# Kernel tuning notes

Hardware: AMD Instinct MI355X
Metric: run time of the kernel (lower is better)

## Reference

```python
import jax, jax.numpy as jnp
import numpy as np

N = 50000      # nodes
E = 800000     # edges (before self loops)
F_IN = 512     # input feature dim (num_features)
D = 128        # hidden_dim
NBLK = 3       # num_layers - 1
EPS = 1e-5


def _layernorm(x, g, b):
    mu = x.mean(-1, keepdims=True)
    var = ((x - mu) ** 2).mean(-1, keepdims=True)
    return (x - mu) / jnp.sqrt(var + EPS) * g + b


def _gatv2(x, Wl, bl, Wr, br, att, bias, src, dst, n):
    # PyG GATv2Conv, heads=1, eval mode (attention dropout off), self loops in src/dst
    xl = x @ Wl + bl                      # [N, D] messages (x_j side)
    xr = x @ Wr + br                      # [N, D] target side (x_i)
    e = jax.nn.leaky_relu(xl[src] + xr[dst], negative_slope=0.2)  # [E', D]
    score = e @ att                       # [E']
    smax = jax.ops.segment_max(score, dst, num_segments=n)
    ex = jnp.exp(score - smax[dst])
    denom = jax.ops.segment_sum(ex, dst, num_segments=n)
    alpha = ex / denom[dst]               # segment softmax over incoming edges
    out = jax.ops.segment_sum(alpha[:, None] * xl[src], dst, num_segments=n)
    return out + bias


def setup_inputs() -> dict:
    key = jax.random.key(0)
    ks = jax.random.split(key, 32)
    w = lambda k, shape: (jax.random.normal(k, shape, jnp.float32) * 0.02)
    p = {}
    p["x"] = jax.random.normal(ks[0], (N, F_IN), jnp.float32)
    p["edge_index"] = jax.random.randint(ks[1], (2, E), 0, N)
    p["emb_W"] = w(ks[2], (F_IN, D)); p["emb_b"] = jnp.zeros((D,), jnp.float32)
    p["ln1_g"] = jnp.ones((NBLK, D), jnp.float32); p["ln1_b"] = jnp.zeros((NBLK, D), jnp.float32)
    p["gat_Wl"] = w(ks[3], (NBLK, D, D)); p["gat_bl"] = jnp.zeros((NBLK, D), jnp.float32)
    p["gat_Wr"] = w(ks[4], (NBLK, D, D)); p["gat_br"] = jnp.zeros((NBLK, D), jnp.float32)
    p["gat_att"] = w(ks[5], (NBLK, D)); p["gat_bias"] = jnp.zeros((NBLK, D), jnp.float32)
    for i in range(NBLK):
        h = D * (i + 1)  # mlp_ratio = level = i+1
        p[f"mlp_w1_{i}"] = w(ks[6 + 2 * i], (D, h))
        p[f"mlp_w2_{i}"] = w(ks[7 + 2 * i], (h, D))
    p["attn_Wa"] = w(ks[12], (D, D)); p["attn_ba"] = jnp.zeros((D,), jnp.float32)
    p["attn_Wb"] = w(ks[13], (D, D)); p["attn_bb"] = jnp.zeros((D,), jnp.float32)
    p["attn_Wc"] = w(ks[14], (D, 1)); p["attn_bc"] = jnp.zeros((1,), jnp.float32)
    p["rho_W"] = w(ks[15], (D, D)); p["rho_b"] = jnp.zeros((D,), jnp.float32)
    p["cls_W"] = w(ks[16], (D, 4)); p["cls_b"] = jnp.zeros((4,), jnp.float32)
    return p


def reference(x, edge_index, emb_W, emb_b, ln1_g, ln1_b, gat_Wl, gat_bl, gat_Wr, gat_br,
              gat_att, gat_bias, mlp_w1_0, mlp_w2_0, mlp_w1_1, mlp_w2_1, mlp_w1_2, mlp_w2_2,
              attn_Wa, attn_ba, attn_Wb, attn_bb, attn_Wc, attn_bc, rho_W, rho_b, cls_W, cls_b):
    n = x.shape[0]
    sl = jnp.arange(n, dtype=edge_index.dtype)
    src = jnp.concatenate([edge_index[0], sl])  # add self loops (GATv2Conv default)
    dst = jnp.concatenate([edge_index[1], sl])
    h = jax.nn.relu(x @ emb_W + emb_b)          # embedding (dropout off)
    mlps = [(mlp_w1_0, mlp_w2_0), (mlp_w1_1, mlp_w2_1), (mlp_w1_2, mlp_w2_2)]
    for i in range(NBLK):
        hn = _layernorm(h, ln1_g[i], ln1_b[i])
        h = h + _gatv2(hn, gat_Wl[i], gat_bl[i], gat_Wr[i], gat_br[i], gat_att[i], gat_bias[i], src, dst, n)
        w1, w2 = mlps[i]
        # NOTE: original forward applies channel_mix directly on x (norm2 is unused)
        h = h + jax.nn.gelu(h @ w1, approximate=False) @ w2
    # Attn_Net_Gated pooling
    a = jnp.tanh(h @ attn_Wa + attn_ba)
    b = jax.nn.sigmoid(h @ attn_Wb + attn_bb)
    A = ((a * b) @ attn_Wc + attn_bc).T          # [1, N]
    h_path = jax.nn.softmax(A, axis=1) @ h       # [1, D]
    hr = jax.nn.relu(h_path @ rho_W + rho_b)
    logits = hr @ cls_W + cls_b                  # [1, 4]
    Y_hat = jnp.argmax(logits, axis=1, keepdims=True)
    hazards = jax.nn.sigmoid(logits)
    S = jnp.cumprod(1.0 - hazards, axis=1)
    return (hazards, S, Y_hat, logits)
```

## Files before the change

### kernel.cpp

```cpp
#include <hip/hip_runtime.h>
#include <math.h>


#define D 128
#define NBLK 3

typedef __attribute__((ext_vector_type(8))) short bf16x8;
typedef __attribute__((ext_vector_type(4))) float f32x4;

static __device__ __forceinline__ float wred_sum(float v) {
#pragma unroll
    for (int m = 1; m < 64; m <<= 1) v += __shfl_xor(v, m, 64);
    return v;
}

static __device__ __forceinline__ float bf2f(unsigned short u) {
    union { unsigned i; float f; } c; c.i = ((unsigned)u) << 16; return c.f;
}
static __device__ __forceinline__ unsigned short f2bf(float f) {
    union { float f; unsigned i; } c; c.f = f;
    unsigned r = c.i + 0x7fff + ((c.i >> 16) & 1);
    return (unsigned short)(r >> 16);
}

static __device__ __forceinline__ void gl16(const unsigned short* g, unsigned short* l) {
    __builtin_amdgcn_global_load_lds((const __attribute__((address_space(1))) void*)g,
                                     (__attribute__((address_space(3))) void*)l, 16, 0, 0);
}

__global__ void zero_k(int* deg, int* fill, float* red, int n) {
    int i = blockIdx.x * blockDim.x + threadIdx.x;
    if (i < n) { deg[i] = 0; fill[i] = 0; }
    if (i < 132) red[i] = 0.f;
}

__global__ void hist_k(const int* __restrict__ dst, int* __restrict__ deg, int E) {
    int e = blockIdx.x * blockDim.x + threadIdx.x;
    if (e < E) atomicAdd(&deg[dst[e]], 1);
}

__global__ __launch_bounds__(256) void blockscan_k(const int* __restrict__ deg,
                                                   int* __restrict__ rowptr,
                                                   int* __restrict__ bsum, int n) {
    __shared__ int tmp[256];
    const int tid = threadIdx.x;
    const int i = blockIdx.x * 256 + tid;
    int v = (i < n) ? deg[i] : 0;
    tmp[tid] = v;
    __syncthreads();
#pragma unroll
    for (int off = 1; off < 256; off <<= 1) {
        int t = (tid >= off) ? tmp[tid - off] : 0;
        __syncthreads();
        tmp[tid] += t;
        __syncthreads();
    }
    if (i < n) rowptr[i + 1] = tmp[tid];
    if (tid == 255) bsum[blockIdx.x] = tmp[255];
}

__global__ __launch_bounds__(256) void scansums_k(int* __restrict__ bsum, int nb) {
    __shared__ int tmp[256];
    const int tid = threadIdx.x;
    int v = (tid < nb) ? bsum[tid] : 0;
    tmp[tid] = v;
    __syncthreads();
#pragma unroll
    for (int off = 1; off < 256; off <<= 1) {
        int t = (tid >= off) ? tmp[tid - off] : 0;
        __syncthreads();
        tmp[tid] += t;
        __syncthreads();
    }
    if (tid < nb) bsum[tid] = tmp[tid];
}

__global__ __launch_bounds__(256) void addoff_k(int* __restrict__ rowptr,
                                                const int* __restrict__ bsum, int n) {
    int i = blockIdx.x * 256 + threadIdx.x;
    if (i == 0) rowptr[0] = 0;
    if (i < n && blockIdx.x > 0) rowptr[i + 1] += bsum[blockIdx.x - 1];
}

__global__ void scatter_k(const int* __restrict__ src, const int* __restrict__ dst,
                          const int* __restrict__ rowptr, int* __restrict__ fill,
                          int* __restrict__ esrc, int E) {
    int e = blockIdx.x * blockDim.x + threadIdx.x;
    if (e < E) {
        int d = dst[e];
        int pos = rowptr[d] + atomicAdd(&fill[d], 1);
        esrc[pos] = src[e];
    }
}

struct WDesc { const float* s; unsigned short* d; int K; int M; };
struct WPack { WDesc w[16]; };

__global__ __launch_bounds__(256) void wprep_k(WPack p) {
    WDesc d = p.w[blockIdx.y];
    const int nc = d.K / 32;
    const int chunks = (d.M / 16) * nc * 64;
    for (int i = blockIdx.x * 256 + threadIdx.x; i < chunks; i += gridDim.x * 256) {
        const int l = i & 63;
        const int c = (i >> 6) % nc;
        const int t = i / (64 * nc);
        const int m = t * 16 + (l & 15);
        const int kb = c * 32 + ((l >> 4) & 3) * 8;
#pragma unroll
        for (int j = 0; j < 8; ++j)
            d.d[(size_t)i * 8 + j] = f2bf(d.s[(size_t)(kb + j) * d.M + m]);
    }
}

__global__ __launch_bounds__(256) void bcat_k(const float* bl, const float* br,
                                              const float* ba, const float* bb,
                                              float* sb) {
    const int t = threadIdx.x;
    for (int i = 0; i < 3; ++i)
        sb[i * 256 + t] = (t < 128) ? bl[i * 128 + t] : br[i * 128 + t - 128];
    sb[3 * 256 + t] = (t < 128) ? ba[t] : bb[t - 128];
}

template <int TK, int TBN, int ACT, bool BIAS, bool ACC, bool LNM, bool A16,
          bool W32, bool W16>
__global__ __launch_bounds__(256) void rgemm_k(const void* __restrict__ Ap,
                                               const unsigned short* __restrict__ BTc,
                                               const float* __restrict__ bias,
                                               const float* __restrict__ lng,
                                               const float* __restrict__ lnb,
                                               float* __restrict__ C32,
                                               unsigned short* __restrict__ C16,
                                               int N, int strideA, int koff, int M) {
    constexpr int NC = TK / 32;
    constexpr int NT = TBN / 16;
    __shared__ unsigned short Bls[TBN * TK];
    const int tid = threadIdx.x;
    const int w = tid >> 6, l = tid & 63;
    const int q = l >> 4;

    const unsigned short* bsrc = BTc + (size_t)blockIdx.y * (NT * NC * 512);
    constexpr int ITER = (TBN * TK / 8) / 256;
#pragma unroll
    for (int i = 0; i < ITER; ++i) {
        const int idx = i * 256 + tid;
        gl16(bsrc + (size_t)idx * 8, &Bls[idx * 8]);
    }

    int r = blockIdx.x * 64 + w * 16 + (l & 15);
    if (r > N - 1) r = N - 1;
    bf16x8 afr[NC];
    if (A16) {
        const unsigned short* A = (const unsigned short*)Ap;
#pragma unroll
        for (int c = 0; c < NC; ++c)
            afr[c] = *(const bf16x8*)(A + (size_t)r * strideA + koff + c * 32 + q * 8);
    } else {
        const float* A = (const float*)Ap;
        float av[NC][8];
#pragma unroll
        for (int c = 0; c < NC; ++c) {
            const float* ap = A + (size_t)r * strideA + koff + c * 32 + q * 8;
            const float4 v0 = *(const float4*)ap;
            const float4 v1 = *(const float4*)(ap + 4);
            av[c][0] = v0.x; av[c][1] = v0.y; av[c][2] = v0.z; av[c][3] = v0.w;
            av[c][4] = v1.x; av[c][5] = v1.y; av[c][6] = v1.z; av[c][7] = v1.w;
        }
        if (LNM) {
            float s = 0.f;
#pragma unroll
            for (int c = 0; c < NC; ++c)
#pragma unroll
                for (int j = 0; j < 8; ++j) s += av[c][j];
            s += __shfl_xor(s, 16, 64); s += __shfl_xor(s, 32, 64);
            const float mu = s * (1.f / (float)TK);
            float vv = 0.f;
#pragma unroll
            for (int c = 0; c < NC; ++c)
#pragma unroll
                for (int j = 0; j < 8; ++j) { const float dd = av[c][j] - mu; vv += dd * dd; }
            vv += __shfl_xor(vv, 16, 64); vv += __shfl_xor(vv, 32, 64);
            const float rs = rsqrtf(vv * (1.f / (float)TK) + 1e-5f);
#pragma unroll
            for (int c = 0; c < NC; ++c) {
                const int kb = c * 32 + q * 8;
                const float4 g0 = *(const float4*)(lng + kb);
                const float4 g1 = *(const float4*)(lng + kb + 4);
                const float4 b0 = *(const float4*)(lnb + kb);
                const float4 b1 = *(const float4*)(lnb + kb + 4);
                const float gg[8] = {g0.x, g0.y, g0.z, g0.w, g1.x, g1.y, g1.z, g1.w};
                const float bbv[8] = {b0.x, b0.y, b0.z, b0.w, b1.x, b1.y, b1.z, b1.w};
#pragma unroll
                for (int j = 0; j < 8; ++j)
                    av[c][j] = (av[c][j] - mu) * rs * gg[j] + bbv[j];
            }
        }
#pragma unroll
        for (int c = 0; c < NC; ++c)
#pragma unroll
            for (int j = 0; j < 8; ++j) afr[c][j] = (short)f2bf(av[c][j]);
    }

    f32x4 acc[NT];
#pragma unroll
    for (int t = 0; t < NT; ++t) acc[t] = (f32x4){0.f, 0.f, 0.f, 0.f};

    __syncthreads();

#pragma unroll
    for (int c = 0; c < NC; ++c)
#pragma unroll
        for (int t = 0; t < NT; ++t) {
            const bf16x8 bfr = *(const bf16x8*)&Bls[((t * NC + c) * 64 + l) * 8];
            acc[t] = __builtin_amdgcn_mfma_f32_16x16x32_bf16(afr[c], bfr, acc[t], 0, 0, 0);
        }

    const int col0 = blockIdx.y * TBN;
    const int rb = blockIdx.x * 64 + w * 16 + q * 4;
#pragma unroll
    for (int t = 0; t < NT; ++t) {
        const int col = col0 + t * 16 + (l & 15);
        const float bv = BIAS ? bias[col] : 0.f;
#pragma unroll
        for (int rr = 0; rr < 4; ++rr) {
            const int row = rb + rr;
            if (row >= N) continue;
            float xv = acc[t][rr] + bv;
            if (ACC) xv += C32[(size_t)row * M + col];
            if (ACT == 1) xv = fmaxf(xv, 0.f);
            else if (ACT == 2) xv = 0.5f * xv * (1.f + erff(xv * 0.70710678118654752f));
            else if (ACT == 5) xv = (col < 128) ? tanhf(xv) : 1.f / (1.f + expf(-xv));
            if (W32) C32[(size_t)row * M + col] = xv;
            if (W16) C16[(size_t)row * M + col] = f2bf(xv);
        }
    }
}

__global__ __launch_bounds__(256) void gat3_k(const unsigned short* __restrict__ X,
                                              const float* __restrict__ att,
                                              const float* __restrict__ gbias,
                                              const int* __restrict__ rowptr,
                                              const int* __restrict__ esrc,
                                              float* __restrict__ H, int n) {
    const int l = threadIdx.x & 63;
    const int node = blockIdx.x * 4 + (threadIdx.x >> 6);
    if (node >= n) return;
    const int q = l >> 4;
    const int d0 = (l & 15) * 8;

    float a8[8], xr[8], xs[8];
    {
        const float4 t0 = *(const float4*)&att[d0];
        const float4 t1 = *(const float4*)&att[d0 + 4];
        a8[0] = t0.x; a8[1] = t0.y; a8[2] = t0.z; a8[3] = t0.w;
        a8[4] = t1.x; a8[5] = t1.y; a8[6] = t1.z; a8[7] = t1.w;
        const bf16x8 uxs = *(const bf16x8*)&X[(size_t)node * 256 + d0];
        const bf16x8 uxr = *(const bf16x8*)&X[(size_t)node * 256 + 128 + d0];
#pragma unroll
        for (int j = 0; j < 8; ++j) {
            xs[j] = bf2f((unsigned short)uxs[j]);
            xr[j] = bf2f((unsigned short)uxr[j]);
        }
    }

    float sc = 0.f;
#pragma unroll
    for (int j = 0; j < 8; ++j) {
        const float e = xs[j] + xr[j];
        sc = fmaf(a8[j], fmaxf(e, 0.2f * e), sc);
    }
#pragma unroll
    for (int m = 1; m < 16; m <<= 1) sc += __shfl_xor(sc, m, 64);
    const float wself = __expf(sc);
    float dsum = (q == 0) ? wself : 0.f;
    float acc[8];
#pragma unroll
    for (int j = 0; j < 8; ++j) acc[j] = (q == 0) ? wself * xs[j] : 0.f;

    const int p0 = rowptr[node], p1 = rowptr[node + 1];
    for (int p = p0 + q; p < p1; p += 4) {
        const int s = esrc[p];
        const bf16x8 ux = *(const bf16x8*)&X[(size_t)s * 256 + d0];
        float xl[8];
#pragma unroll
        for (int j = 0; j < 8; ++j) xl[j] = bf2f((unsigned short)ux[j]);
        float e_sc = 0.f;
#pragma unroll
        for (int j = 0; j < 8; ++j) {
            const float e = xl[j] + xr[j];
            e_sc = fmaf(a8[j], fmaxf(e, 0.2f * e), e_sc);
        }
#pragma unroll
        for (int m = 1; m < 16; m <<= 1) e_sc += __shfl_xor(e_sc, m, 64);
        const float wgt = __expf(e_sc);
        dsum += wgt;
#pragma unroll
        for (int j = 0; j < 8; ++j) acc[j] = fmaf(wgt, xl[j], acc[j]);
    }

#pragma unroll
    for (int m = 16; m < 64; m <<= 1) {
        dsum += __shfl_xor(dsum, m, 64);
#pragma unroll
        for (int j = 0; j < 8; ++j) acc[j] += __shfl_xor(acc[j], m, 64);
    }

    if (q == 0) {
        const float inv = 1.f / dsum;
        const size_t o = (size_t)node * D + d0;
        float4 h0 = *(const float4*)&H[o];
        float4 h1 = *(const float4*)&H[o + 4];
        float hv[8] = {h0.x, h0.y, h0.z, h0.w, h1.x, h1.y, h1.z, h1.w};
#pragma unroll
        for (int j = 0; j < 8; ++j) hv[j] += acc[j] * inv + gbias[d0 + j];
        *(float4*)&H[o]     = make_float4(hv[0], hv[1], hv[2], hv[3]);
        *(float4*)&H[o + 4] = make_float4(hv[4], hv[5], hv[6], hv[7]);
    }
}

__global__ __launch_bounds__(256) void poolA_k(const float* __restrict__ P,
                                               const float* __restrict__ Wc,
                                               const float* __restrict__ bc,
                                               float* __restrict__ A, int n) {
    const int lane = threadIdx.x & 63;
    const int node = blockIdx.x * 4 + (threadIdx.x >> 6);
    if (node >= n) return;
    const size_t o = (size_t)node * 256;
    const float v = wred_sum(P[o + lane] * P[o + 128 + lane] * Wc[lane] +
                             P[o + 64 + lane] * P[o + 192 + lane] * Wc[64 + lane]);
    if (lane == 0) A[node] = v + bc[0];
}

__global__ __launch_bounds__(256) void wsum_k(const float* __restrict__ A,
                                              const float* __restrict__ H,
                                              float* __restrict__ red, int n) {
    const int lane = threadIdx.x & 63;
    const int gw = blockIdx.x * 4 + (threadIdx.x >> 6);
    const int nw = gridDim.x * 4;
    float a0 = 0.f, a1 = 0.f, dn = 0.f;
    for (int node = gw; node < n; node += nw) {
        const float w = __expf(A[node]);
        dn += w;
        a0 = fmaf(w, H[(size_t)node * D + lane], a0);
        a1 = fmaf(w, H[(size_t)node * D + 64 + lane], a1);
    }
    atomicAdd(&red[lane], a0);
    atomicAdd(&red[64 + lane], a1);
    if (lane == 0) atomicAdd(&red[128], dn);
}

__global__ __launch_bounds__(128) void final_k(const float* __restrict__ red,
                                               const float* __restrict__ rho_W,
                                               const float* __restrict__ rho_b,
                                               const float* __restrict__ cls_W,
                                               const float* __restrict__ cls_b,
                                               float* __restrict__ out) {
    __shared__ float hp[128];
    __shared__ float hr[128];
    __shared__ float lg[4];
    const int t = threadIdx.x;
    hp[t] = red[t] / red[128];
    __syncthreads();
    float s = rho_b[t];
    for (int k = 0; k < 128; ++k) s = fmaf(hp[k], rho_W[k * 128 + t], s);
    hr[t] = fmaxf(s, 0.f);
    __syncthreads();
    if (t < 4) {
        float l = cls_b[t];
        for (int k = 0; k < 128; ++k) l = fmaf(hr[k], cls_W[k * 4 + t], l);
        lg[t] = l;
    }
    __syncthreads();
    if (t == 0) {
        float hz[4], S[4];
        for (int c = 0; c < 4; ++c) hz[c] = 1.f / (1.f + expf(-lg[c]));
        S[0] = 1.f - hz[0];
        for (int c = 1; c < 4; ++c) S[c] = S[c - 1] * (1.f - hz[c]);
        int am = 0; float bm = lg[0];
        for (int c = 1; c < 4; ++c) if (lg[c] > bm) { bm = lg[c]; am = c; }
        out[0] = hz[0]; out[1] = hz[1]; out[2] = hz[2]; out[3] = hz[3];
        out[4] = S[0];  out[5] = S[1];  out[6] = S[2];  out[7] = S[3];
        out[8] = (float)am;
        out[9] = lg[0]; out[10] = lg[1]; out[11] = lg[2]; out[12] = lg[3];
    }
}

static inline int cdiv(int a, int b) { return (a + b - 1) / b; }

extern "C" void kernel_launch(void* const* d_in, const int* in_sizes, int n_in,
                              void* d_out, int out_size, void* d_ws, size_t ws_size,
                              hipStream_t stream) {
    const float* x      = (const float*)d_in[0];
    const int*   ei     = (const int*)d_in[1];
    const float* emb_W  = (const float*)d_in[2];
    const float* emb_b  = (const float*)d_in[3];
    const float* ln1_g  = (const float*)d_in[4];
    const float* ln1_b  = (const float*)d_in[5];
    const float* gat_Wl = (const float*)d_in[6];
    const float* gat_bl = (const float*)d_in[7];
    const float* gat_Wr = (const float*)d_in[8];
    const float* gat_br = (const float*)d_in[9];
    const float* gat_att  = (const float*)d_in[10];
    const float* gat_bias = (const float*)d_in[11];
    const float* mlp_w1[NBLK] = {(const float*)d_in[12], (const float*)d_in[14], (const float*)d_in[16]};
    const float* mlp_w2[NBLK] = {(const float*)d_in[13], (const float*)d_in[15], (const float*)d_in[17]};
    const float* attn_Wa = (const float*)d_in[18];
    const float* attn_ba = (const float*)d_in[19];
    const float* attn_Wb = (const float*)d_in[20];
    const float* attn_bb = (const float*)d_in[21];
    const float* attn_Wc = (const float*)d_in[22];
    const float* attn_bc = (const float*)d_in[23];
    const float* rho_W   = (const float*)d_in[24];
    const float* rho_b   = (const float*)d_in[25];
    const float* cls_W   = (const float*)d_in[26];
    const float* cls_b   = (const float*)d_in[27];
    float* out = (float*)d_out;

    const int N = in_sizes[0] / 512;
    const int E = in_sizes[1] / 2;
    const int* src = ei;
    const int* dst = ei + E;

    char* base = (char*)d_ws;
    float* P = (float*)base;
    float* H = P + (size_t)N * 256;
    unsigned short* X = (unsigned short*)(H + (size_t)N * D);
    unsigned short* T = X + (size_t)N * 256;
    float* Avec = (float*)(T + (size_t)N * 384);
    float* red  = Avec + N;
    float* sb   = red + 132;
    unsigned short* wbuf = (unsigned short*)(sb + 1024);
    int* esrc   = (int*)(wbuf + 393216);
    int* deg    = esrc + E;
    int* rowptr = deg + N;
    int* fill   = rowptr + N + 1;
    int* bsum   = fill + N;

    unsigned short* embT = wbuf;
    unsigned short* gatT = wbuf + 65536;
    unsigned short* w1T0 = gatT + 3 * 32768;
    unsigned short* w1T1 = w1T0 + 16384;
    unsigned short* w1T2 = w1T1 + 32768;
    unsigned short* w2T0 = w1T2 + 49152;
    unsigned short* w2T1 = w2T0 + 16384;
    unsigned short* w2T2 = w2T1 + 32768;
    unsigned short* attT = w2T2 + 49152;
    unsigned short* w1T[NBLK] = {w1T0, w1T1, w1T2};
    unsigned short* w2T[NBLK] = {w2T0, w2T1, w2T2};

    const int nb = cdiv(N, 256);
    zero_k<<<cdiv(N, 256), 256, 0, stream>>>(deg, fill, red, N);
    hist_k<<<cdiv(E, 256), 256, 0, stream>>>(dst, deg, E);
    blockscan_k<<<nb, 256, 0, stream>>>(deg, rowptr, bsum, N);
    scansums_k<<<1, 256, 0, stream>>>(bsum, nb);
    addoff_k<<<nb, 256, 0, stream>>>(rowptr, bsum, N);
    scatter_k<<<cdiv(E, 256), 256, 0, stream>>>(src, dst, rowptr, fill, esrc, E);

    {
        WPack p;
        p.w[0] = {emb_W,             embT,         256, 128};
        p.w[1] = {emb_W + 256 * 128, embT + 32768, 256, 128};
        for (int i = 0; i < 3; ++i) {
            p.w[2 + i] = {gat_Wl + (size_t)i * 16384, gatT + (size_t)i * 32768,         128, 128};
            p.w[5 + i] = {gat_Wr + (size_t)i * 16384, gatT + (size_t)i * 32768 + 16384, 128, 128};
            p.w[8 + i]  = {mlp_w1[i], w1T[i], 128, 128 * (i + 1)};
            p.w[11 + i] = {mlp_w2[i], w2T[i], 128 * (i + 1), 128};
        }
        p.w[14] = {attn_Wa, attT,         128, 128};
        p.w[15] = {attn_Wb, attT + 16384, 128, 128};
        wprep_k<<<dim3(64, 16), 256, 0, stream>>>(p);
    }
    bcat_k<<<1, 256, 0, stream>>>(gat_bl, gat_br, attn_ba, attn_bb, sb);

    const int gx = cdiv(N, 64);

    rgemm_k<256, 128, 0, false, false, false, false, true, false>
        <<<dim3(gx, 1), 256, 0, stream>>>(x, embT, nullptr, nullptr, nullptr,
                                          H, nullptr, N, 512, 0, 128);
    rgemm_k<256, 128, 1, true, true, false, false, true, false>
        <<<dim3(gx, 1), 256, 0, stream>>>(x, embT + 32768, emb_b, nullptr, nullptr,
                                          H, nullptr, N, 512, 256, 128);

    for (int i = 0; i < NBLK; ++i) {
        rgemm_k<128, 128, 0, true, false, true, false, false, true>
            <<<dim3(gx, 2), 256, 0, stream>>>(H, gatT + (size_t)i * 32768, sb + i * 256,
                                              ln1_g + i * D, ln1_b + i * D,
                                              nullptr, X, N, 128, 0, 256);
        gat3_k<<<cdiv(N, 4), 256, 0, stream>>>(X, gat_att + i * D, gat_bias + i * D,
                                               rowptr, esrc, H, N);
        const int h = D * (i + 1);
        rgemm_k<128, 128, 2, false, false, false, false, false, true>
            <<<dim3(gx, i + 1), 256, 0, stream>>>(H, w1T[i], nullptr, nullptr, nullptr,
                                                  nullptr, T, N, 128, 0, h);
        if (i == 0)
            rgemm_k<128, 128, 0, false, true, false, true, true, false>
                <<<dim3(gx, 1), 256, 0, stream>>>(T, w2T[i], nullptr, nullptr, nullptr,
                                                  H, nullptr, N, h, 0, 128);
        else if (i == 1)
            rgemm_k<256, 128, 0, false, true, false, true, true, false>
                <<<dim3(gx, 1), 256, 0, stream>>>(T, w2T[i], nullptr, nullptr, nullptr,
                                                  H, nullptr, N, h, 0, 128);
        else
            rgemm_k<384, 64, 0, false, true, false, true, true, false>
                <<<dim3(gx, 2), 256, 0, stream>>>(T, w2T[i], nullptr, nullptr, nullptr,
                                                  H, nullptr, N, h, 0, 128);
    }

    rgemm_k<128, 128, 5, true, false, false, false, true, false>
        <<<dim3(gx, 2), 256, 0, stream>>>(H, attT, sb + 3 * 256, nullptr, nullptr,
                                          P, nullptr, N, 128, 0, 256);
    poolA_k<<<cdiv(N, 4), 256, 0, stream>>>(P, attn_Wc, attn_bc, Avec, N);
    wsum_k<<<120, 256, 0, stream>>>(Avec, H, red, N);
    final_k<<<1, 128, 0, stream>>>(red, rho_W, rho_b, cls_W, cls_b, out);
}
```

Measured before the change: 772.0 us.

## Loop GEMM over 128x128 weight rounds, prefetch GAT gathers, fuse pooling kernels

The GEMM kernel now iterates over 128x128 weight tiles inside one block. It accumulates over K rounds or walks output column rounds, so each block loads its A rows once and the embedding GEMM becomes a single launch instead of two. The GAT aggregation loop software-pipelines the neighbor feature gathers two edges ahead to hide gather latency. The pooling score and weighted-sum kernels are fused, which drops the intermediate A vector and one launch. In exchange, grids are smaller (one block per 64 rows), which lowers parallelism, and each round adds syncthreads and a serialized shared-memory reload.

```diff
diff --git a/kernel.cpp b/kernel.cpp
--- a/kernel.cpp
+++ b/kernel.cpp
@@ -94,7 +94,7 @@
 }
 
 struct WDesc { const float* s; unsigned short* d; int K; int M; };
-struct WPack { WDesc w[16]; };
+struct WPack { WDesc w[21]; };
 
 __global__ __launch_bounds__(256) void wprep_k(WPack p) {
     WDesc d = p.w[blockIdx.y];
@@ -121,7 +121,7 @@
     sb[3 * 256 + t] = (t < 128) ? ba[t] : bb[t - 128];
 }
 
-template <int TK, int TBN, int ACT, bool BIAS, bool ACC, bool LNM, bool A16,
+template <int NR, bool KM, int ACT, bool BIAS, bool ACC, bool LNM, bool A16,
           bool W32, bool W16>
 __global__ __launch_bounds__(256) void rgemm_k(const void* __restrict__ Ap,
                                                const unsigned short* __restrict__ BTc,
@@ -130,109 +130,120 @@
                                                const float* __restrict__ lnb,
                                                float* __restrict__ C32,
                                                unsigned short* __restrict__ C16,
-                                               int N, int strideA, int koff, int M) {
-    constexpr int NC = TK / 32;
-    constexpr int NT = TBN / 16;
-    __shared__ unsigned short Bls[TBN * TK];
+                                               int N, int strideA, int M) {
+    __shared__ unsigned short Bls[128 * 128];
     const int tid = threadIdx.x;
     const int w = tid >> 6, l = tid & 63;
     const int q = l >> 4;
-
-    const unsigned short* bsrc = BTc + (size_t)blockIdx.y * (NT * NC * 512);
-    constexpr int ITER = (TBN * TK / 8) / 256;
-#pragma unroll
-    for (int i = 0; i < ITER; ++i) {
-        const int idx = i * 256 + tid;
-        gl16(bsrc + (size_t)idx * 8, &Bls[idx * 8]);
-    }
-
     int r = blockIdx.x * 64 + w * 16 + (l & 15);
     if (r > N - 1) r = N - 1;
-    bf16x8 afr[NC];
-    if (A16) {
-        const unsigned short* A = (const unsigned short*)Ap;
-#pragma unroll
-        for (int c = 0; c < NC; ++c)
-            afr[c] = *(const bf16x8*)(A + (size_t)r * strideA + koff + c * 32 + q * 8);
-    } else {
-        const float* A = (const float*)Ap;
-        float av[NC][8];
-#pragma unroll
-        for (int c = 0; c < NC; ++c) {
-            const float* ap = A + (size_t)r * strideA + koff + c * 32 + q * 8;
-            const float4 v0 = *(const float4*)ap;
-            const float4 v1 = *(const float4*)(ap + 4);
-            av[c][0] = v0.x; av[c][1] = v0.y; av[c][2] = v0.z; av[c][3] = v0.w;
-            av[c][4] = v1.x; av[c][5] = v1.y; av[c][6] = v1.z; av[c][7] = v1.w;
-        }
-        if (LNM) {
-            float s = 0.f;
-#pragma unroll
-            for (int c = 0; c < NC; ++c)
-#pragma unroll
-                for (int j = 0; j < 8; ++j) s += av[c][j];
-            s += __shfl_xor(s, 16, 64); s += __shfl_xor(s, 32, 64);
-            const float mu = s * (1.f / (float)TK);
-            float vv = 0.f;
-#pragma unroll
-            for (int c = 0; c < NC; ++c)
-#pragma unroll
-                for (int j = 0; j < 8; ++j) { const float dd = av[c][j] - mu; vv += dd * dd; }
-            vv += __shfl_xor(vv, 16, 64); vv += __shfl_xor(vv, 32, 64);
-            const float rs = rsqrtf(vv * (1.f / (float)TK) + 1e-5f);
-#pragma unroll
-            for (int c = 0; c < NC; ++c) {
-                const int kb = c * 32 + q * 8;
-                const float4 g0 = *(const float4*)(lng + kb);
-                const float4 g1 = *(const float4*)(lng + kb + 4);
-                const float4 b0 = *(const float4*)(lnb + kb);
-                const float4 b1 = *(const float4*)(lnb + kb + 4);
-                const float gg[8] = {g0.x, g0.y, g0.z, g0.w, g1.x, g1.y, g1.z, g1.w};
-                const float bbv[8] = {b0.x, b0.y, b0.z, b0.w, b1.x, b1.y, b1.z, b1.w};
-#pragma unroll
-                for (int j = 0; j < 8; ++j)
-                    av[c][j] = (av[c][j] - mu) * rs * gg[j] + bbv[j];
+
+    bf16x8 afr[4];
+    auto loadA = [&](int koff) {
+        if (A16) {
+            const unsigned short* A = (const unsigned short*)Ap;
+#pragma unroll
+            for (int c = 0; c < 4; ++c)
+                afr[c] = *(const bf16x8*)(A + (size_t)r * strideA + koff + c * 32 + q * 8);
+        } else {
+            const float* A = (const float*)Ap;
+            float av[4][8];
+#pragma unroll
+            for (int c = 0; c < 4; ++c) {
+                const float* ap = A + (size_t)r * strideA + koff + c * 32 + q * 8;
+                const float4 v0 = *(const float4*)ap;
+                const float4 v1 = *(const float4*)(ap + 4);
+                av[c][0] = v0.x; av[c][1] = v0.y; av[c][2] = v0.z; av[c][3] = v0.w;
+                av[c][4] = v1.x; av[c][5] = v1.y; av[c][6] = v1.z; av[c][7] = v1.w;
             }
-        }
-#pragma unroll
-        for (int c = 0; c < NC; ++c)
-#pragma unroll
-            for (int j = 0; j < 8; ++j) afr[c][j] = (short)f2bf(av[c][j]);
-    }
-
-    f32x4 acc[NT];
-#pragma unroll
-    for (int t = 0; t < NT; ++t) acc[t] = (f32x4){0.f, 0.f, 0.f, 0.f};
-
-    __syncthreads();
-
-#pragma unroll
-    for (int c = 0; c < NC; ++c)
-#pragma unroll
-        for (int t = 0; t < NT; ++t) {
-            const bf16x8 bfr = *(const bf16x8*)&Bls[((t * NC + c) * 64 + l) * 8];
-            acc[t] = __builtin_amdgcn_mfma_f32_16x16x32_bf16(afr[c], bfr, acc[t], 0, 0, 0);
-        }
-
-    const int col0 = blockIdx.y * TBN;
+            if (LNM) {
+                float s = 0.f;
+#pragma unroll
+                for (int c = 0; c < 4; ++c)
+#pragma unroll
+                    for (int j = 0; j < 8; ++j) s += av[c][j];
+                s += __shfl_xor(s, 16, 64); s += __shfl_xor(s, 32, 64);
+                const float mu = s * (1.f / 128.f);
+                float vv = 0.f;
+#pragma unroll
+                for (int c = 0; c < 4; ++c)
+#pragma unroll
+                    for (int j = 0; j < 8; ++j) { const float dd = av[c][j] - mu; vv += dd * dd; }
+                vv += __shfl_xor(vv, 16, 64); vv += __shfl_xor(vv, 32, 64);
+                const float rs = rsqrtf(vv * (1.f / 128.f) + 1e-5f);
+#pragma unroll
+                for (int c = 0; c < 4; ++c) {
+                    const int kb = c * 32 + q * 8;
+                    const float4 g0 = *(const float4*)(lng + kb);
+                    const float4 g1 = *(const float4*)(lng + kb + 4);
+                    const float4 b0 = *(const float4*)(lnb + kb);
+                    const float4 b1 = *(const float4*)(lnb + kb + 4);
+                    const float gg[8] = {g0.x, g0.y, g0.z, g0.w, g1.x, g1.y, g1.z, g1.w};
+                    const float bb[8] = {b0.x, b0.y, b0.z, b0.w, b1.x, b1.y, b1.z, b1.w};
+#pragma unroll
+                    for (int j = 0; j < 8; ++j)
+                        av[c][j] = (av[c][j] - mu) * rs * gg[j] + bb[j];
+                }
+            }
+#pragma unroll
+            for (int c = 0; c < 4; ++c)
+#pragma unroll
+                for (int j = 0; j < 8; ++j) afr[c][j] = (short)f2bf(av[c][j]);
+        }
+    };
+
+    f32x4 acc[8];
+#pragma unroll
+    for (int t = 0; t < 8; ++t) acc[t] = (f32x4){0.f, 0.f, 0.f, 0.f};
+
+    if (!KM) loadA(0);
+
     const int rb = blockIdx.x * 64 + w * 16 + q * 4;
-#pragma unroll
-    for (int t = 0; t < NT; ++t) {
-        const int col = col0 + t * 16 + (l & 15);
-        const float bv = BIAS ? bias[col] : 0.f;
-#pragma unroll
-        for (int rr = 0; rr < 4; ++rr) {
-            const int row = rb + rr;
-            if (row >= N) continue;
-            float xv = acc[t][rr] + bv;
-            if (ACC) xv += C32[(size_t)row * M + col];
-            if (ACT == 1) xv = fmaxf(xv, 0.f);
-            else if (ACT == 2) xv = 0.5f * xv * (1.f + erff(xv * 0.70710678118654752f));
-            else if (ACT == 5) xv = (col < 128) ? tanhf(xv) : 1.f / (1.f + expf(-xv));
-            if (W32) C32[(size_t)row * M + col] = xv;
-            if (W16) C16[(size_t)row * M + col] = f2bf(xv);
-        }
-    }
+    auto epi = [&](int col0) {
+#pragma unroll
+        for (int t = 0; t < 8; ++t) {
+            const int col = col0 + t * 16 + (l & 15);
+            const float bv = BIAS ? bias[col] : 0.f;
+#pragma unroll
+            for (int rr = 0; rr < 4; ++rr) {
+                const int row = rb + rr;
+                if (row >= N) continue;
+                float xv = acc[t][rr] + bv;
+                if (ACC) xv += C32[(size_t)row * M + col];
+                if (ACT == 1) xv = fmaxf(xv, 0.f);
+                else if (ACT == 2) xv = 0.5f * xv * (1.f + erff(xv * 0.70710678118654752f));
+                else if (ACT == 5) xv = (col < 128) ? tanhf(xv) : 1.f / (1.f + expf(-xv));
+                if (W32) C32[(size_t)row * M + col] = xv;
+                if (W16) C16[(size_t)row * M + col] = f2bf(xv);
+            }
+        }
+    };
+
+#pragma unroll
+    for (int rnd = 0; rnd < NR; ++rnd) {
+        if (rnd) __syncthreads();
+        const unsigned short* bsrc = BTc + (size_t)rnd * 16384;
+#pragma unroll
+        for (int i = 0; i < 8; ++i) {
+            const int idx = i * 256 + tid;
+            gl16(bsrc + (size_t)idx * 8, &Bls[idx * 8]);
+        }
+        if (KM) loadA(rnd * 128);
+        __syncthreads();
+#pragma unroll
+        for (int c = 0; c < 4; ++c)
+#pragma unroll
+            for (int t = 0; t < 8; ++t) {
+                const bf16x8 bfr = *(const bf16x8*)&Bls[((t * 4 + c) * 64 + l) * 8];
+                acc[t] = __builtin_amdgcn_mfma_f32_16x16x32_bf16(afr[c], bfr, acc[t], 0, 0, 0);
+            }
+        if (!KM) {
+            epi(rnd * 128);
+#pragma unroll
+            for (int t = 0; t < 8; ++t) acc[t] = (f32x4){0.f, 0.f, 0.f, 0.f};
+        }
+    }
+    if (KM) epi(0);
 }
 
 __global__ __launch_bounds__(256) void gat3_k(const unsigned short* __restrict__ X,
@@ -276,13 +287,22 @@
 #pragma unroll
     for (int j = 0; j < 8; ++j) acc[j] = (q == 0) ? wself * xs[j] : 0.f;
 
-    const int p0 = rowptr[node], p1 = rowptr[node + 1];
-    for (int p = p0 + q; p < p1; p += 4) {
-        const int s = esrc[p];
-        const bf16x8 ux = *(const bf16x8*)&X[(size_t)s * 256 + d0];
+    const int p1 = rowptr[node + 1];
+    int p = rowptr[node] + q;
+    bool v0 = p < p1, v1 = p + 4 < p1, v2 = p + 8 < p1;
+    int i2 = v2 ? esrc[p + 8] : 0;
+    bf16x8 u0, u1;
+    if (v0) u0 = *(const bf16x8*)&X[(size_t)esrc[p] * 256 + d0];
+    if (v1) u1 = *(const bf16x8*)&X[(size_t)esrc[p + 4] * 256 + d0];
+    while (v0) {
+        bf16x8 u2;
+        if (v2) u2 = *(const bf16x8*)&X[(size_t)i2 * 256 + d0];
+        const bool v3 = p + 12 < p1;
+        const int i3 = v3 ? esrc[p + 12] : 0;
+
         float xl[8];
 #pragma unroll
-        for (int j = 0; j < 8; ++j) xl[j] = bf2f((unsigned short)ux[j]);
+        for (int j = 0; j < 8; ++j) xl[j] = bf2f((unsigned short)u0[j]);
         float e_sc = 0.f;
 #pragma unroll
         for (int j = 0; j < 8; ++j) {
@@ -295,6 +315,10 @@
         dsum += wgt;
 #pragma unroll
         for (int j = 0; j < 8; ++j) acc[j] = fmaf(wgt, xl[j], acc[j]);
+
+        u0 = u1; u1 = u2; i2 = i3;
+        v0 = v1; v1 = v2; v2 = v3;
+        p += 4;
     }
 
 #pragma unroll
@@ -317,31 +341,25 @@
     }
 }
 
-__global__ __launch_bounds__(256) void poolA_k(const float* __restrict__ P,
-                                               const float* __restrict__ Wc,
-                                               const float* __restrict__ bc,
-                                               float* __restrict__ A, int n) {
-    const int lane = threadIdx.x & 63;
-    const int node = blockIdx.x * 4 + (threadIdx.x >> 6);
-    if (node >= n) return;
-    const size_t o = (size_t)node * 256;
-    const float v = wred_sum(P[o + lane] * P[o + 128 + lane] * Wc[lane] +
-                             P[o + 64 + lane] * P[o + 192 + lane] * Wc[64 + lane]);
-    if (lane == 0) A[node] = v + bc[0];
-}
-
-__global__ __launch_bounds__(256) void wsum_k(const float* __restrict__ A,
-                                              const float* __restrict__ H,
-                                              float* __restrict__ red, int n) {
+__global__ __launch_bounds__(256) void poolws_k(const float* __restrict__ P,
+                                                const float* __restrict__ Wc,
+                                                const float* __restrict__ bc,
+                                                const float* __restrict__ H,
+                                                float* __restrict__ red, int n) {
     const int lane = threadIdx.x & 63;
     const int gw = blockIdx.x * 4 + (threadIdx.x >> 6);
     const int nw = gridDim.x * 4;
+    const float wc0 = Wc[lane], wc1 = Wc[64 + lane];
+    const float bcv = bc[0];
     float a0 = 0.f, a1 = 0.f, dn = 0.f;
     for (int node = gw; node < n; node += nw) {
-        const float w = __expf(A[node]);
-        dn += w;
-        a0 = fmaf(w, H[(size_t)node * D + lane], a0);
-        a1 = fmaf(w, H[(size_t)node * D + 64 + lane], a1);
+        const size_t o = (size_t)node * 256;
+        const float v = wred_sum(P[o + lane] * P[o + 128 + lane] * wc0 +
+                                 P[o + 64 + lane] * P[o + 192 + lane] * wc1);
+        const float wgt = __expf(v + bcv);
+        dn += wgt;
+        a0 = fmaf(wgt, H[(size_t)node * D + lane], a0);
+        a1 = fmaf(wgt, H[(size_t)node * D + 64 + lane], a1);
     }
     atomicAdd(&red[lane], a0);
     atomicAdd(&red[64 + lane], a1);
@@ -425,8 +443,7 @@
     float* H = P + (size_t)N * 256;
     unsigned short* X = (unsigned short*)(H + (size_t)N * D);
     unsigned short* T = X + (size_t)N * 256;
-    float* Avec = (float*)(T + (size_t)N * 384);
-    float* red  = Avec + N;
+    float* red  = (float*)(T + (size_t)N * 384);
     float* sb   = red + 132;
     unsigned short* wbuf = (unsigned short*)(sb + 1024);
     int* esrc   = (int*)(wbuf + 393216);
@@ -436,14 +453,14 @@
     int* bsum   = fill + N;
 
     unsigned short* embT = wbuf;
-    unsigned short* gatT = wbuf + 65536;
-    unsigned short* w1T0 = gatT + 3 * 32768;
+    unsigned short* gatT = wbuf + 4 * 16384;
+    unsigned short* w1T0 = gatT + 6 * 16384;
     unsigned short* w1T1 = w1T0 + 16384;
-    unsigned short* w1T2 = w1T1 + 32768;
-    unsigned short* w2T0 = w1T2 + 49152;
+    unsigned short* w1T2 = w1T1 + 2 * 16384;
+    unsigned short* w2T0 = w1T2 + 3 * 16384;
     unsigned short* w2T1 = w2T0 + 16384;
-    unsigned short* w2T2 = w2T1 + 32768;
-    unsigned short* attT = w2T2 + 49152;
+    unsigned short* w2T2 = w2T1 + 2 * 16384;
+    unsigned short* attT = w2T2 + 3 * 16384;
     unsigned short* w1T[NBLK] = {w1T0, w1T1, w1T2};
     unsigned short* w2T[NBLK] = {w2T0, w2T1, w2T2};
 
@@ -457,58 +474,66 @@
 
     {
         WPack p;
-        p.w[0] = {emb_W,             embT,         256, 128};
-        p.w[1] = {emb_W + 256 * 128, embT + 32768, 256, 128};
+        int di = 0;
+        for (int r = 0; r < 4; ++r)
+            p.w[di++] = {emb_W + (size_t)r * 128 * 128, embT + (size_t)r * 16384, 128, 128};
         for (int i = 0; i < 3; ++i) {
-            p.w[2 + i] = {gat_Wl + (size_t)i * 16384, gatT + (size_t)i * 32768,         128, 128};
-            p.w[5 + i] = {gat_Wr + (size_t)i * 16384, gatT + (size_t)i * 32768 + 16384, 128, 128};
-            p.w[8 + i]  = {mlp_w1[i], w1T[i], 128, 128 * (i + 1)};
-            p.w[11 + i] = {mlp_w2[i], w2T[i], 128 * (i + 1), 128};
-        }
-        p.w[14] = {attn_Wa, attT,         128, 128};
-        p.w[15] = {attn_Wb, attT + 16384, 128, 128};
-        wprep_k<<<dim3(64, 16), 256, 0, stream>>>(p);
+            p.w[di++] = {gat_Wl + (size_t)i * 16384, gatT + (size_t)(2 * i) * 16384, 128, 128};
+            p.w[di++] = {gat_Wr + (size_t)i * 16384, gatT + (size_t)(2 * i + 1) * 16384, 128, 128};
+        }
+        for (int i = 0; i < 3; ++i)
+            p.w[di++] = {mlp_w1[i], w1T[i], 128, 128 * (i + 1)};
+        for (int i = 0; i < 3; ++i)
+            for (int r = 0; r <= i; ++r)
+                p.w[di++] = {mlp_w2[i] + (size_t)r * 128 * 128, w2T[i] + (size_t)r * 16384, 128, 128};
+        p.w[di++] = {attn_Wa, attT, 128, 128};
+        p.w[di++] = {attn_Wb, attT + 16384, 128, 128};
+        wprep_k<<<dim3(32, 21), 256, 0, stream>>>(p);
     }
     bcat_k<<<1, 256, 0, stream>>>(gat_bl, gat_br, attn_ba, attn_bb, sb);
 
     const int gx = cdiv(N, 64);
 
-    rgemm_k<256, 128, 0, false, false, false, false, true, false>
-        <<<dim3(gx, 1), 256, 0, stream>>>(x, embT, nullptr, nullptr, nullptr,
-                                          H, nullptr, N, 512, 0, 128);
-    rgemm_k<256, 128, 1, true, true, false, false, true, false>
-        <<<dim3(gx, 1), 256, 0, stream>>>(x, embT + 32768, emb_b, nullptr, nullptr,
-                                          H, nullptr, N, 512, 256, 128);
+    rgemm_k<4, true, 1, true, false, false, false, true, false>
+        <<<gx, 256, 0, stream>>>(x, embT, emb_b, nullptr, nullptr,
+                                 H, nullptr, N, 512, 128);
 
     for (int i = 0; i < NBLK; ++i) {
-        rgemm_k<128, 128, 0, true, false, true, false, false, true>
-            <<<dim3(gx, 2), 256, 0, stream>>>(H, gatT + (size_t)i * 32768, sb + i * 256,
-                                              ln1_g + i * D, ln1_b + i * D,
-                                              nullptr, X, N, 128, 0, 256);
+        rgemm_k<2, false, 0, true, false, true, false, false, true>
+            <<<gx, 256, 0, stream>>>(H, gatT + (size_t)(2 * i) * 16384, sb + i * 256,
+                                     ln1_g + i * D, ln1_b + i * D, nullptr, X, N, 128, 256);
         gat3_k<<<cdiv(N, 4), 256, 0, stream>>>(X, gat_att + i * D, gat_bias + i * D,
                                                rowptr, esrc, H, N);
         const int h = D * (i + 1);
-        rgemm_k<128, 128, 2, false, false, false, false, false, true>
-            <<<dim3(gx, i + 1), 256, 0, stream>>>(H, w1T[i], nullptr, nullptr, nullptr,
-                                                  nullptr, T, N, 128, 0, h);
         if (i == 0)
-            rgemm_k<128, 128, 0, false, true, false, true, true, false>
-                <<<dim3(gx, 1), 256, 0, stream>>>(T, w2T[i], nullptr, nullptr, nullptr,
-                                                  H, nullptr, N, h, 0, 128);
+            rgemm_k<1, false, 2, false, false, false, false, false, true>
+                <<<gx, 256, 0, stream>>>(H, w1T[i], nullptr, nullptr, nullptr,
+                                         nullptr, T, N, 128, h);
         else if (i == 1)
-            rgemm_k<256, 128, 0, false, true, false, true, true, false>
-                <<<dim3(gx, 1), 256, 0, stream>>>(T, w2T[i], nullptr, nullptr, nullptr,
-                                                  H, nullptr, N, h, 0, 128);
+            rgemm_k<2, false, 2, false, false, false, false, false, true>
+                <<<gx, 256, 0, stream>>>(H, w1T[i], nullptr, nullptr, nullptr,
+                                         nullptr, T, N, 128, h);
         else
-            rgemm_k<384, 64, 0, false, true, false, true, true, false>
-                <<<dim3(gx, 2), 256, 0, stream>>>(T, w2T[i], nullptr, nullptr, nullptr,
-                                                  H, nullptr, N, h, 0, 128);
-    }
-
-    rgemm_k<128, 128, 5, true, false, false, false, true, false>
-        <<<dim3(gx, 2), 256, 0, stream>>>(H, attT, sb + 3 * 256, nullptr, nullptr,
-                                          P, nullptr, N, 128, 0, 256);
-    poolA_k<<<cdiv(N, 4), 256, 0, stream>>>(P, attn_Wc, attn_bc, Avec, N);
-    wsum_k<<<120, 256, 0, stream>>>(Avec, H, red, N);
+            rgemm_k<3, false, 2, false, false, false, false, false, true>
+                <<<gx, 256, 0, stream>>>(H, w1T[i], nullptr, nullptr, nullptr,
+                                         nullptr, T, N, 128, h);
+        if (i == 0)
+            rgemm_k<1, true, 0, false, true, false, true, true, false>
+                <<<gx, 256, 0, stream>>>(T, w2T[i], nullptr, nullptr, nullptr,
+                                         H, nullptr, N, h, 128);
+        else if (i == 1)
+            rgemm_k<2, true, 0, false, true, false, true, true, false>
+                <<<gx, 256, 0, stream>>>(T, w2T[i], nullptr, nullptr, nullptr,
+                                         H, nullptr, N, h, 128);
+        else
+            rgemm_k<3, true, 0, false, true, false, true, true, false>
+                <<<gx, 256, 0, stream>>>(T, w2T[i], nullptr, nullptr, nullptr,
+                                         H, nullptr, N, h, 128);
+    }
+
+    rgemm_k<2, false, 5, true, false, false, false, true, false>
+        <<<gx, 256, 0, stream>>>(H, attT, sb + 3 * 256, nullptr, nullptr,
+                                 P, nullptr, N, 128, 256);
+    poolws_k<<<120, 256, 0, stream>>>(P, attn_Wc, attn_bc, H, red, N);
     final_k<<<1, 128, 0, stream>>>(red, rho_W, rho_b, cls_W, cls_b, out);
 }
```

Result: faster. 748.2 us (-3.1%).
